# Kernel tuning notes

Measured on AMD Instinct MI355X. Metric: run time of the kernel, lower is better.

## Reference

```python
import jax, jax.numpy as jnp
import numpy as np

K = 1  # top-k from init_kwargs


def setup_inputs() -> dict:
    key = jax.random.key(0)
    k0, k1, k2, k3, k4, k5 = jax.random.split(key, 6)
    B, L, Ed, NE = 8192, 1024, 1024, 8
    D = L + Ed  # input_dim = latent_dim + embed_dim
    s = 1.0 / np.sqrt(D)  # torch nn.Linear default init bound
    x = jax.random.normal(k0, (B, L), dtype=jnp.float32)
    y = jax.random.normal(k1, (B, Ed), dtype=jnp.float32)
    We = jax.random.uniform(k2, (NE, D, D), dtype=jnp.float32, minval=-s, maxval=s)  # expert weights [E, out, in]
    be = jax.random.uniform(k3, (NE, D), dtype=jnp.float32, minval=-s, maxval=s)
    gW = jax.random.uniform(k4, (NE, D), dtype=jnp.float32, minval=-s, maxval=s)  # gate weight [E, in]
    gb = jax.random.uniform(k5, (NE,), dtype=jnp.float32, minval=-s, maxval=s)
    return {"x": x, "y": y, "We": We, "be": be, "gW": gW, "gb": gb}


def reference(x, y, We, be, gW, gb):
    # inp: [B, D]
    inp = jnp.concatenate([x, y], axis=1)
    # gate logits: [B, E] (eval mode: no noise)
    gate_logits = inp @ gW.T + gb
    topk_val, topk_idx = jax.lax.top_k(gate_logits, K)  # [B, K]
    topk_gates = jax.nn.softmax(topk_val, axis=1)       # [B, K]
    # dense compute-all-experts (faithful to original): [B, E, D]
    all_out = jnp.einsum('bd,eod->beo', inp, We) + be[None, :, :]
    # gather top-k experts per token: [B, K, D]
    gathered = jnp.take_along_axis(all_out, topk_idx[:, :, None], axis=1)
    fused = jnp.sum(gathered * topk_gates[:, :, None], axis=1)  # [B, D]
    return fused
```

## Files before the change

### kernel.cpp

```cpp
#include <hip/hip_runtime.h>
#include <stdint.h>

#define B_TOK 8192
#define DIM   2048
#define NE    8
#define BM 128
#define BN 128
#define BK 64

typedef __bf16 bf16x8 __attribute__((ext_vector_type(8)));
typedef float  f32x4  __attribute__((ext_vector_type(4)));

__device__ __forceinline__ unsigned short f2b(float f) {
  unsigned u = __builtin_bit_cast(unsigned, f);
  u += 0x7fffu + ((u >> 16) & 1u);
  return (unsigned short)(u >> 16);
}
__device__ __forceinline__ uint2 pack4(float4 v) {
  uint2 r;
  r.x = (unsigned)f2b(v.x) | ((unsigned)f2b(v.y) << 16);
  r.y = (unsigned)f2b(v.z) | ((unsigned)f2b(v.w) << 16);
  return r;
}
__device__ __forceinline__ void gload16(const void* g, void* l) {
  __builtin_amdgcn_global_load_lds(
      (const __attribute__((address_space(1))) void*)g,
      (__attribute__((address_space(3))) void*)l, 16, 0, 0);
}

__global__ __launch_bounds__(256) void cvt_we(const float* __restrict__ src,
                                              unsigned short* __restrict__ dst) {
  size_t idx = (size_t)blockIdx.x * 256 + threadIdx.x;
  float4 v = *(const float4*)(src + idx * 4);
  *(uint2*)(dst + idx * 4) = pack4(v);
}

template <bool WINP>
__global__ void gate_kernel(const float* __restrict__ x,
                            const float* __restrict__ y,
                            const float* __restrict__ gW,
                            const float* __restrict__ gb,
                            int* __restrict__ eid,
                            unsigned short* __restrict__ inpB) {
  const int tid = threadIdx.x;
  const int ln = tid & 63;
  const int token = blockIdx.x * 4 + (tid >> 6);

  double acc[NE];
#pragma unroll
  for (int e = 0; e < NE; ++e) acc[e] = 0.0;

  const float* bases[2] = {x, y};
#pragma unroll
  for (int p = 0; p < 2; ++p) {
    const float* rowp = bases[p] + (size_t)token * 1024;
#pragma unroll
    for (int it = 0; it < 4; ++it) {
      const int d = it * 256 + ln * 4;
      float4 v = *(const float4*)(rowp + d);
      if (WINP)
        *(uint2*)(inpB + (size_t)token * DIM + p * 1024 + d) = pack4(v);
#pragma unroll
      for (int e = 0; e < NE; ++e) {
        float4 g = *(const float4*)(gW + e * DIM + p * 1024 + d);
        acc[e] += (double)v.x * (double)g.x + (double)v.y * (double)g.y +
                  (double)v.z * (double)g.z + (double)v.w * (double)g.w;
      }
    }
  }
#pragma unroll
  for (int e = 0; e < NE; ++e) {
#pragma unroll
    for (int off = 32; off >= 1; off >>= 1) acc[e] += __shfl_xor(acc[e], off, 64);
  }
  if (ln == 0) {
    int best = 0;
    double bv = acc[0] + (double)gb[0];
#pragma unroll
    for (int e = 1; e < NE; ++e) {
      double v = acc[e] + (double)gb[e];
      if (v > bv) { bv = v; best = e; }
    }
    eid[token] = best;
  }
}

__global__ __launch_bounds__(256) void bucketize(const int* __restrict__ eid,
                                                 int* __restrict__ counts,
                                                 int* __restrict__ perm) {
  const int e = blockIdx.x;
  const int tid = threadIdx.x, ln = tid & 63, wv = tid >> 6;
  __shared__ int wsum[4];
  __shared__ int basev;
  if (tid == 0) basev = 0;
  __syncthreads();
  for (int t0 = 0; t0 < B_TOK; t0 += 256) {
    int t = t0 + tid;
    bool m = (eid[t] == e);
    unsigned long long mk = __ballot(m);
    int pre = __popcll(mk & ((1ull << ln) - 1ull));
    if (ln == 0) wsum[wv] = __popcll(mk);
    __syncthreads();
    int off = basev;
    for (int w = 0; w < wv; ++w) off += wsum[w];
    if (m) perm[e * B_TOK + off + pre] = t;
    __syncthreads();
    if (tid == 0) basev += wsum[0] + wsum[1] + wsum[2] + wsum[3];
    __syncthreads();
  }
  if (tid == 0) counts[e] = basev;
}

template <bool PRE>
__global__ __launch_bounds__(256) void moe_gemm(
    const float* __restrict__ x,
    const float* __restrict__ y,
    const float* __restrict__ We,
    const float* __restrict__ be,
    const unsigned short* __restrict__ inpB,
    const unsigned short* __restrict__ WeB,
    const int* __restrict__ counts,
    const int* __restrict__ perm,
    float* __restrict__ out) {
  __shared__ unsigned short As[BM * BK];
  __shared__ unsigned short Bs[BN * BK];
  __shared__ int tokLds[BM];

  const int e = blockIdx.z;
  const int cnt = counts[e];
  const int m0 = blockIdx.y * BM;
  if (m0 >= cnt) return;
  const int n0 = blockIdx.x * BN;

  const int tid = threadIdx.x;
  const int ln = tid & 63;
  const int wv = tid >> 6;
  const int wm = wv & 1, wn = wv >> 1;

  if (tid < BM) {
    int r = m0 + tid;
    tokLds[tid] = perm[e * B_TOK + (r < cnt ? r : cnt - 1)];
  }
  __syncthreads();

  const int cS = (ln & 7) ^ ((ln >> 3) & 7);
  int tokA[4], rowB[4];
#pragma unroll
  for (int j = 0; j < 4; ++j) {
    int row = (wv * 4 + j) * 8 + (ln >> 3);
    tokA[j] = tokLds[row];
    rowB[j] = row;
  }
  const unsigned short* wbbase = WeB + (size_t)e * DIM * DIM;
  const float* wfbase = We + (size_t)e * DIM * DIM;

  f32x4 acc[4][4];
#pragma unroll
  for (int i = 0; i < 4; ++i)
#pragma unroll
    for (int j = 0; j < 4; ++j) acc[i][j] = (f32x4){0.f, 0.f, 0.f, 0.f};

  for (int k0 = 0; k0 < DIM; k0 += BK) {
    __syncthreads();
    if constexpr (PRE) {
#pragma unroll
      for (int j = 0; j < 4; ++j) {
        gload16(inpB + (size_t)tokA[j] * DIM + k0 + cS * 8,
                &As[(wv * 4 + j) * 512]);
        gload16(wbbase + (size_t)(n0 + rowB[j]) * DIM + k0 + cS * 8,
                &Bs[(wv * 4 + j) * 512]);
      }
    } else {
      const float* ab = (k0 < 1024) ? x : y;
      const int kk = k0 & 1023;
#pragma unroll
      for (int i = 0; i < 8; ++i) {
        int li = i * 256 + tid;
        int row = li >> 4, k4 = li & 15;
        int ksl = (k4 & 7) ^ (row & 7);
        int chunk = k4 >> 1, half = k4 & 1;
        int slot = (chunk ^ (row & 7)) * 2 + half;
        int tok = tokLds[row];
        float4 va = *(const float4*)(ab + (size_t)tok * 1024 + kk + k4 * 4);
        *(uint2*)&As[row * BK + slot * 4] = pack4(va);
        float4 vb = *(const float4*)(wfbase + (size_t)(n0 + row) * DIM + k0 + k4 * 4);
        *(uint2*)&Bs[row * BK + slot * 4] = pack4(vb);
        (void)ksl;
      }
    }
    __syncthreads();

#pragma unroll
    for (int ks = 0; ks < 2; ++ks) {
      bf16x8 av[4], bv[4];
#pragma unroll
      for (int i = 0; i < 4; ++i) {
        int rA = wm * 64 + i * 16 + (ln & 15);
        int c = ks * 4 + (ln >> 4);
        av[i] = *(const bf16x8*)&As[rA * BK + (c ^ (rA & 7)) * 8];
      }
#pragma unroll
      for (int j = 0; j < 4; ++j) {
        int rB = wn * 64 + j * 16 + (ln & 15);
        int c = ks * 4 + (ln >> 4);
        bv[j] = *(const bf16x8*)&Bs[rB * BK + (c ^ (rB & 7)) * 8];
      }
#pragma unroll
      for (int i = 0; i < 4; ++i)
#pragma unroll
        for (int j = 0; j < 4; ++j)
          acc[i][j] = __builtin_amdgcn_mfma_f32_16x16x32_bf16(av[i], bv[j], acc[i][j], 0, 0, 0);
    }
  }

  float bias[4]; int col[4];
#pragma unroll
  for (int j = 0; j < 4; ++j) {
    col[j] = n0 + wn * 64 + j * 16 + (ln & 15);
    bias[j] = be[e * DIM + col[j]];
  }
#pragma unroll
  for (int i = 0; i < 4; ++i) {
    int rbase = wm * 64 + i * 16 + ((ln >> 4) << 2);
#pragma unroll
    for (int r = 0; r < 4; ++r) {
      int rl = rbase + r;
      if (m0 + rl < cnt) {
        size_t t = (size_t)tokLds[rl];
#pragma unroll
        for (int j = 0; j < 4; ++j)
          out[t * DIM + col[j]] = acc[i][j][r] + bias[j];
      }
    }
  }
}

extern "C" void kernel_launch(void* const* d_in, const int* in_sizes, int n_in,
                              void* d_out, int out_size, void* d_ws, size_t ws_size,
                              hipStream_t stream) {
  const float* x  = (const float*)d_in[0];
  const float* y  = (const float*)d_in[1];
  const float* We = (const float*)d_in[2];
  const float* be = (const float*)d_in[3];
  const float* gW = (const float*)d_in[4];
  const float* gb = (const float*)d_in[5];
  float* out = (float*)d_out;

  char* ws = (char*)d_ws;
  int* counts = (int*)ws;
  int* eid    = (int*)(ws + 256);
  int* perm   = (int*)(ws + 33024);
  unsigned short* inpB = (unsigned short*)(ws + 295168);
  unsigned short* WeB  = (unsigned short*)(ws + 33849600);
  const size_t needed = 33849600ull + 67108864ull;

  if (ws_size >= needed) {
    gate_kernel<true><<<dim3(B_TOK / 4), 256, 0, stream>>>(x, y, gW, gb, eid, inpB);
    cvt_we<<<dim3(32768), 256, 0, stream>>>(We, WeB);
    bucketize<<<dim3(NE), 256, 0, stream>>>(eid, counts, perm);
    moe_gemm<true><<<dim3(DIM / BN, B_TOK / BM, NE), 256, 0, stream>>>(
        x, y, We, be, inpB, WeB, counts, perm, out);
  } else {
    gate_kernel<false><<<dim3(B_TOK / 4), 256, 0, stream>>>(x, y, gW, gb, eid, nullptr);
    bucketize<<<dim3(NE), 256, 0, stream>>>(eid, counts, perm);
    moe_gemm<false><<<dim3(DIM / BN, B_TOK / BM, NE), 256, 0, stream>>>(
        x, y, We, be, nullptr, nullptr, counts, perm, out);
  }
}
```

Baseline: 431.3 us.

## Fuse gate and weight conversion into one prepass; persistent M-tile loop in GEMM

Merges the gating kernel and the expert-weight bf16 conversion into one launch: extra blocks convert We with 16-byte stores while the first 2048 blocks do gating. The gating loop is also rewritten as a single non-unrolled loop. The MoE GEMM grid shrinks from one block per M tile to a fixed 8 blocks in y, each looping over M tiles with stride 8. This removes a launch and the many empty blocks that exited early for small experts. The cost is less parallelism when one expert gets many tokens, since each block then processes its tiles serially.

```diff
diff --git a/kernel.cpp b/kernel.cpp
--- a/kernel.cpp
+++ b/kernel.cpp
@@ -7,6 +7,7 @@
 #define BM 128
 #define BN 128
 #define BK 64
+#define MG 8
 
 typedef __bf16 bf16x8 __attribute__((ext_vector_type(8)));
 typedef float  f32x4  __attribute__((ext_vector_type(4)));
@@ -28,44 +29,47 @@
       (__attribute__((address_space(3))) void*)l, 16, 0, 0);
 }
 
-__global__ __launch_bounds__(256) void cvt_we(const float* __restrict__ src,
-                                              unsigned short* __restrict__ dst) {
-  size_t idx = (size_t)blockIdx.x * 256 + threadIdx.x;
-  float4 v = *(const float4*)(src + idx * 4);
-  *(uint2*)(dst + idx * 4) = pack4(v);
-}
-
 template <bool WINP>
-__global__ void gate_kernel(const float* __restrict__ x,
-                            const float* __restrict__ y,
-                            const float* __restrict__ gW,
-                            const float* __restrict__ gb,
-                            int* __restrict__ eid,
-                            unsigned short* __restrict__ inpB) {
+__global__ __launch_bounds__(256) void prepass(
+    const float* __restrict__ x, const float* __restrict__ y,
+    const float* __restrict__ gW, const float* __restrict__ gb,
+    const float* __restrict__ We,
+    int* __restrict__ eid, unsigned short* __restrict__ inpB,
+    unsigned short* __restrict__ WeB) {
+  const int bid = blockIdx.x;
   const int tid = threadIdx.x;
+  if (WINP && bid >= 2048) {
+    size_t base = (size_t)(bid - 2048) * 2048 + (size_t)tid * 8;
+    float4 v0 = *(const float4*)(We + base);
+    float4 v1 = *(const float4*)(We + base + 4);
+    uint2 a = pack4(v0), b = pack4(v1);
+    uint4 r; r.x = a.x; r.y = a.y; r.z = b.x; r.w = b.y;
+    *(uint4*)(WeB + base) = r;
+    return;
+  }
   const int ln = tid & 63;
-  const int token = blockIdx.x * 4 + (tid >> 6);
+  const int token = bid * 4 + (tid >> 6);
 
   double acc[NE];
 #pragma unroll
   for (int e = 0; e < NE; ++e) acc[e] = 0.0;
 
-  const float* bases[2] = {x, y};
-#pragma unroll
-  for (int p = 0; p < 2; ++p) {
-    const float* rowp = bases[p] + (size_t)token * 1024;
-#pragma unroll
-    for (int it = 0; it < 4; ++it) {
-      const int d = it * 256 + ln * 4;
-      float4 v = *(const float4*)(rowp + d);
-      if (WINP)
-        *(uint2*)(inpB + (size_t)token * DIM + p * 1024 + d) = pack4(v);
-#pragma unroll
-      for (int e = 0; e < NE; ++e) {
-        float4 g = *(const float4*)(gW + e * DIM + p * 1024 + d);
-        acc[e] += (double)v.x * (double)g.x + (double)v.y * (double)g.y +
-                  (double)v.z * (double)g.z + (double)v.w * (double)g.w;
-      }
+  const float* rowx = x + (size_t)token * 1024;
+  const float* rowy = y + (size_t)token * 1024;
+
+#pragma unroll 1
+  for (int it = 0; it < 8; ++it) {
+    const int d = it * 256 + ln * 4;
+    const float* src = (d < 1024) ? (rowx + d) : (rowy + d - 1024);
+    float4 v = *(const float4*)src;
+    if (WINP)
+      *(uint2*)(inpB + (size_t)token * DIM + d) = pack4(v);
+    double vx = v.x, vy = v.y, vz = v.z, vw = v.w;
+#pragma unroll
+    for (int e = 0; e < NE; ++e) {
+      float4 g = *(const float4*)(gW + e * DIM + d);
+      acc[e] += vx * (double)g.x + vy * (double)g.y +
+                vz * (double)g.z + vw * (double)g.w;
     }
   }
 #pragma unroll
@@ -128,90 +132,16 @@
 
   const int e = blockIdx.z;
   const int cnt = counts[e];
-  const int m0 = blockIdx.y * BM;
-  if (m0 >= cnt) return;
   const int n0 = blockIdx.x * BN;
 
   const int tid = threadIdx.x;
   const int ln = tid & 63;
   const int wv = tid >> 6;
   const int wm = wv & 1, wn = wv >> 1;
-
-  if (tid < BM) {
-    int r = m0 + tid;
-    tokLds[tid] = perm[e * B_TOK + (r < cnt ? r : cnt - 1)];
-  }
-  __syncthreads();
-
   const int cS = (ln & 7) ^ ((ln >> 3) & 7);
-  int tokA[4], rowB[4];
-#pragma unroll
-  for (int j = 0; j < 4; ++j) {
-    int row = (wv * 4 + j) * 8 + (ln >> 3);
-    tokA[j] = tokLds[row];
-    rowB[j] = row;
-  }
+
   const unsigned short* wbbase = WeB + (size_t)e * DIM * DIM;
   const float* wfbase = We + (size_t)e * DIM * DIM;
-
-  f32x4 acc[4][4];
-#pragma unroll
-  for (int i = 0; i < 4; ++i)
-#pragma unroll
-    for (int j = 0; j < 4; ++j) acc[i][j] = (f32x4){0.f, 0.f, 0.f, 0.f};
-
-  for (int k0 = 0; k0 < DIM; k0 += BK) {
-    __syncthreads();
-    if constexpr (PRE) {
-#pragma unroll
-      for (int j = 0; j < 4; ++j) {
-        gload16(inpB + (size_t)tokA[j] * DIM + k0 + cS * 8,
-                &As[(wv * 4 + j) * 512]);
-        gload16(wbbase + (size_t)(n0 + rowB[j]) * DIM + k0 + cS * 8,
-                &Bs[(wv * 4 + j) * 512]);
-      }
-    } else {
-      const float* ab = (k0 < 1024) ? x : y;
-      const int kk = k0 & 1023;
-#pragma unroll
-      for (int i = 0; i < 8; ++i) {
-        int li = i * 256 + tid;
-        int row = li >> 4, k4 = li & 15;
-        int ksl = (k4 & 7) ^ (row & 7);
-        int chunk = k4 >> 1, half = k4 & 1;
-        int slot = (chunk ^ (row & 7)) * 2 + half;
-        int tok = tokLds[row];
-        float4 va = *(const float4*)(ab + (size_t)tok * 1024 + kk + k4 * 4);
-        *(uint2*)&As[row * BK + slot * 4] = pack4(va);
-        float4 vb = *(const float4*)(wfbase + (size_t)(n0 + row) * DIM + k0 + k4 * 4);
-        *(uint2*)&Bs[row * BK + slot * 4] = pack4(vb);
-        (void)ksl;
-      }
-    }
-    __syncthreads();
-
-#pragma unroll
-    for (int ks = 0; ks < 2; ++ks) {
-      bf16x8 av[4], bv[4];
-#pragma unroll
-      for (int i = 0; i < 4; ++i) {
-        int rA = wm * 64 + i * 16 + (ln & 15);
-        int c = ks * 4 + (ln >> 4);
-        av[i] = *(const bf16x8*)&As[rA * BK + (c ^ (rA & 7)) * 8];
-      }
-#pragma unroll
-      for (int j = 0; j < 4; ++j) {
-        int rB = wn * 64 + j * 16 + (ln & 15);
-        int c = ks * 4 + (ln >> 4);
-        bv[j] = *(const bf16x8*)&Bs[rB * BK + (c ^ (rB & 7)) * 8];
-      }
-#pragma unroll
-      for (int i = 0; i < 4; ++i)
-#pragma unroll
-        for (int j = 0; j < 4; ++j)
-          acc[i][j] = __builtin_amdgcn_mfma_f32_16x16x32_bf16(av[i], bv[j], acc[i][j], 0, 0, 0);
-    }
-  }
 
   float bias[4]; int col[4];
 #pragma unroll
@@ -219,17 +149,91 @@
     col[j] = n0 + wn * 64 + j * 16 + (ln & 15);
     bias[j] = be[e * DIM + col[j]];
   }
-#pragma unroll
-  for (int i = 0; i < 4; ++i) {
-    int rbase = wm * 64 + i * 16 + ((ln >> 4) << 2);
-#pragma unroll
-    for (int r = 0; r < 4; ++r) {
-      int rl = rbase + r;
-      if (m0 + rl < cnt) {
-        size_t t = (size_t)tokLds[rl];
-#pragma unroll
-        for (int j = 0; j < 4; ++j)
-          out[t * DIM + col[j]] = acc[i][j][r] + bias[j];
+  int rowB[4];
+#pragma unroll
+  for (int j = 0; j < 4; ++j) rowB[j] = (wv * 4 + j) * 8 + (ln >> 3);
+
+  for (int mt = blockIdx.y; mt * BM < cnt; mt += MG) {
+    const int m0 = mt * BM;
+    __syncthreads();
+    if (tid < BM) {
+      int r = m0 + tid;
+      tokLds[tid] = perm[e * B_TOK + (r < cnt ? r : cnt - 1)];
+    }
+    __syncthreads();
+    int tokA[4];
+#pragma unroll
+    for (int j = 0; j < 4; ++j) tokA[j] = tokLds[rowB[j]];
+
+    f32x4 acc[4][4];
+#pragma unroll
+    for (int i = 0; i < 4; ++i)
+#pragma unroll
+      for (int j = 0; j < 4; ++j) acc[i][j] = (f32x4){0.f, 0.f, 0.f, 0.f};
+
+    for (int k0 = 0; k0 < DIM; k0 += BK) {
+      __syncthreads();
+      if constexpr (PRE) {
+#pragma unroll
+        for (int j = 0; j < 4; ++j) {
+          gload16(inpB + (size_t)tokA[j] * DIM + k0 + cS * 8,
+                  &As[(wv * 4 + j) * 512]);
+          gload16(wbbase + (size_t)(n0 + rowB[j]) * DIM + k0 + cS * 8,
+                  &Bs[(wv * 4 + j) * 512]);
+        }
+      } else {
+        const float* ab = (k0 < 1024) ? x : y;
+        const int kk = k0 & 1023;
+#pragma unroll
+        for (int i = 0; i < 8; ++i) {
+          int li = i * 256 + tid;
+          int row = li >> 4, k4 = li & 15;
+          int chunk = k4 >> 1, half = k4 & 1;
+          int slot = (chunk ^ (row & 7)) * 2 + half;
+          int tok = tokLds[row];
+          float4 va = *(const float4*)(ab + (size_t)tok * 1024 + kk + k4 * 4);
+          *(uint2*)&As[row * BK + slot * 4] = pack4(va);
+          float4 vb = *(const float4*)(wfbase + (size_t)(n0 + row) * DIM + k0 + k4 * 4);
+          *(uint2*)&Bs[row * BK + slot * 4] = pack4(vb);
+        }
+      }
+      __syncthreads();
+
+#pragma unroll
+      for (int ks = 0; ks < 2; ++ks) {
+        bf16x8 av[4], bv[4];
+#pragma unroll
+        for (int i = 0; i < 4; ++i) {
+          int rA = wm * 64 + i * 16 + (ln & 15);
+          int c = ks * 4 + (ln >> 4);
+          av[i] = *(const bf16x8*)&As[rA * BK + (c ^ (rA & 7)) * 8];
+        }
+#pragma unroll
+        for (int j = 0; j < 4; ++j) {
+          int rB = wn * 64 + j * 16 + (ln & 15);
+          int c = ks * 4 + (ln >> 4);
+          bv[j] = *(const bf16x8*)&Bs[rB * BK + (c ^ (rB & 7)) * 8];
+        }
+#pragma unroll
+        for (int i = 0; i < 4; ++i)
+#pragma unroll
+          for (int j = 0; j < 4; ++j)
+            acc[i][j] = __builtin_amdgcn_mfma_f32_16x16x32_bf16(av[i], bv[j], acc[i][j], 0, 0, 0);
+      }
+    }
+
+#pragma unroll
+    for (int i = 0; i < 4; ++i) {
+      int rbase = wm * 64 + i * 16 + ((ln >> 4) << 2);
+#pragma unroll
+      for (int r = 0; r < 4; ++r) {
+        int rl = rbase + r;
+        if (m0 + rl < cnt) {
+          size_t t = (size_t)tokLds[rl];
+#pragma unroll
+          for (int j = 0; j < 4; ++j)
+            out[t * DIM + col[j]] = acc[i][j][r] + bias[j];
+        }
       }
     }
   }
@@ -255,15 +259,14 @@
   const size_t needed = 33849600ull + 67108864ull;
 
   if (ws_size >= needed) {
-    gate_kernel<true><<<dim3(B_TOK / 4), 256, 0, stream>>>(x, y, gW, gb, eid, inpB);
-    cvt_we<<<dim3(32768), 256, 0, stream>>>(We, WeB);
+    prepass<true><<<dim3(2048 + 16384), 256, 0, stream>>>(x, y, gW, gb, We, eid, inpB, WeB);
     bucketize<<<dim3(NE), 256, 0, stream>>>(eid, counts, perm);
-    moe_gemm<true><<<dim3(DIM / BN, B_TOK / BM, NE), 256, 0, stream>>>(
+    moe_gemm<true><<<dim3(DIM / BN, MG, NE), 256, 0, stream>>>(
         x, y, We, be, inpB, WeB, counts, perm, out);
   } else {
-    gate_kernel<false><<<dim3(B_TOK / 4), 256, 0, stream>>>(x, y, gW, gb, eid, nullptr);
+    prepass<false><<<dim3(2048), 256, 0, stream>>>(x, y, gW, gb, We, eid, nullptr, nullptr);
     bucketize<<<dim3(NE), 256, 0, stream>>>(eid, counts, perm);
-    moe_gemm<false><<<dim3(DIM / BN, B_TOK / BM, NE), 256, 0, stream>>>(
+    moe_gemm<false><<<dim3(DIM / BN, MG, NE), 256, 0, stream>>>(
         x, y, We, be, nullptr, nullptr, counts, perm, out);
   }
 }
```

After: 432.1 us. Within noise of the previous version (+0.2%).
